# Kernel tuning notes

Measured on AMD Instinct MI355X. Metric: run time of the kernel, lower is better.

The kernel has to match this reference:

```python
import jax, jax.numpy as jnp
import numpy as np

N = 2500   # total_neurons
K = 50     # connections_per_neuron
T = 60     # temporal_sequence
F = 5      # input_features
H = 128    # lstm hidden_size
B = 512    # batch
GROUPS = [800, 700, 600, 400]  # support_resistance, trend_detection, pattern_recognition, volume_analysis


def _lstm_layer(x, Wih, Whh, bih, bhh):
    # x: [B, T, D]; PyTorch gate order (i, f, g, o); eval mode (no dropout)
    bs = x.shape[0]
    h0 = jnp.zeros((bs, H), x.dtype)

    def step(carry, xt):
        h, c = carry
        g = xt @ Wih.T + h @ Whh.T + bih + bhh
        i, f, gg, o = jnp.split(g, 4, axis=-1)
        c = jax.nn.sigmoid(f) * c + jax.nn.sigmoid(i) * jnp.tanh(gg)
        h = jax.nn.sigmoid(o) * jnp.tanh(c)
        return (h, c), h

    (h, c), ys = jax.lax.scan(step, (h0, h0), jnp.swapaxes(x, 0, 1))
    return jnp.swapaxes(ys, 0, 1), h


def _forward(x, W_ih0, W_hh0, b_ih0, b_hh0, W_ih1, W_hh1, b_ih1, b_hh1,
             fp_w1, fp_b1, fp_w2, fp_b2, conn_w, sens, thr,
             int_w1, int_b1, int_w2, int_b2, int_w3, int_b3,
             tw, tb, pw, pb, kw, kb, vw, vb, cw, cb, conn_idx):
    y0, _ = _lstm_layer(x, W_ih0, W_hh0, b_ih0, b_hh0)
    _, hlast = _lstm_layer(y0, W_ih1, W_hh1, b_ih1, b_hh1)        # hidden[-1]: [B, H]
    base = jnp.tanh(jax.nn.relu(hlast @ fp_w1.T + fp_b1) @ fp_w2.T + fp_b2)  # [B, 32]
    # all_activations = base repeated over N neurons; each neuron reduces its
    # K gathered activations (weighted) and the identical 32 feature dims to a scalar.
    feat_sum = base.sum(-1)                                        # [B]
    acts = jnp.broadcast_to(feat_sum[:, None], (x.shape[0], N))    # [B, N]
    gathered = acts[:, conn_idx]                                   # [B, N, K] irregular gather
    wi = jnp.einsum('bnk,nk->bn', gathered, conn_w)                # [B, N]
    pre = wi * sens
    o0 = GROUPS[0]; o1 = o0 + GROUPS[1]; o2 = o1 + GROUPS[2]
    neuron_out = jnp.concatenate([
        jax.nn.sigmoid(pre[:, :o0] - thr[:o0]),                    # support_resistance
        jnp.tanh(pre[:, o0:o1]),                                   # trend_detection
        jax.nn.relu(pre[:, o1:o2] - thr[o1:o2]),                   # pattern_recognition
        jax.nn.sigmoid(pre[:, o2:]),                               # volume_analysis
    ], axis=1)                                                     # [B, N]
    h1 = jax.nn.relu(neuron_out @ int_w1.T + int_b1)
    h2 = jax.nn.relu(h1 @ int_w2.T + int_b2)
    integrated = jnp.tanh(h2 @ int_w3.T + int_b3)                  # [B, 32]
    trend = integrated @ tw.T + tb                                 # [B, 3]
    patt = integrated @ pw.T + pb                                  # [B, 6]
    keyl = integrated @ kw.T + kb                                  # [B, 4]
    vol = integrated @ vw.T + vb                                   # [B, 1]
    conf = integrated @ cw.T + cb                                  # [B, 1]
    means = jnp.stack([neuron_out[:, :o0].mean(1), neuron_out[:, o0:o1].mean(1),
                       neuron_out[:, o1:o2].mean(1), neuron_out[:, o2:].mean(1)], axis=-1)
    # heads(15) + raw confidence(1) + overall_confidence(1) + specialty means(4) -> [B, 21]? no: 3+6+4+1+1+1+4 = 20
    return jnp.concatenate([trend, patt, keyl, vol, conf, jax.nn.sigmoid(conf), means], axis=-1)


def setup_inputs() -> dict:
    key = jax.random.key(0)
    ks = jax.random.split(key, 40)
    rn = lambda k, s, sc=0.1: jax.random.normal(k, s, dtype=jnp.float32) * sc
    inp = {}
    inp['x'] = jax.random.normal(ks[0], (B, T, F), dtype=jnp.float32)
    inp['W_ih0'] = rn(ks[1], (4 * H, F)); inp['W_hh0'] = rn(ks[2], (4 * H, H))
    inp['b_ih0'] = rn(ks[3], (4 * H,));   inp['b_hh0'] = rn(ks[4], (4 * H,))
    inp['W_ih1'] = rn(ks[5], (4 * H, H)); inp['W_hh1'] = rn(ks[6], (4 * H, H))
    inp['b_ih1'] = rn(ks[7], (4 * H,));   inp['b_hh1'] = rn(ks[8], (4 * H,))
    inp['fp_w1'] = rn(ks[9], (64, H));    inp['fp_b1'] = rn(ks[10], (64,))
    inp['fp_w2'] = rn(ks[11], (32, 64));  inp['fp_b2'] = rn(ks[12], (32,))
    inp['conn_w'] = rn(ks[13], (N, K))
    inp['sens'] = 1.0 + rn(ks[14], (N,))
    inp['thr'] = 0.6 + rn(ks[15], (N,))
    inp['int_w1'] = rn(ks[16], (256, N), 0.02); inp['int_b1'] = rn(ks[17], (256,))
    inp['int_w2'] = rn(ks[18], (64, 256));      inp['int_b2'] = rn(ks[19], (64,))
    inp['int_w3'] = rn(ks[20], (32, 64));       inp['int_b3'] = rn(ks[21], (32,))
    inp['tw'] = rn(ks[22], (3, 32)); inp['tb'] = rn(ks[23], (3,))
    inp['pw'] = rn(ks[24], (6, 32)); inp['pb'] = rn(ks[25], (6,))
    inp['kw'] = rn(ks[26], (4, 32)); inp['kb'] = rn(ks[27], (4,))
    inp['vw'] = rn(ks[28], (1, 32)); inp['vb'] = rn(ks[29], (1,))
    inp['cw'] = rn(ks[30], (1, 32)); inp['cb'] = rn(ks[31], (1,))
    inp['conn_idx'] = jax.random.randint(ks[32], (N, K), 0, N)
    return inp


def reference(x, W_ih0, W_hh0, b_ih0, b_hh0, W_ih1, W_hh1, b_ih1, b_hh1,
              fp_w1, fp_b1, fp_w2, fp_b2, conn_w, sens, thr,
              int_w1, int_b1, int_w2, int_b2, int_w3, int_b3,
              tw, tb, pw, pb, kw, kb, vw, vb, cw, cb, conn_idx):
    return _forward(x, W_ih0, W_hh0, b_ih0, b_hh0, W_ih1, W_hh1, b_ih1, b_hh1,
                    fp_w1, fp_b1, fp_w2, fp_b2, conn_w, sens, thr,
                    int_w1, int_b1, int_w2, int_b2, int_w3, int_b3,
                    tw, tb, pw, pb, kw, kb, vw, vb, cw, cb, conn_idx)
```

## Files before the change

kernel.cpp:

```cpp
#include <hip/hip_runtime.h>
#include <math.h>

#define NB   512
#define TT   60
#define FF   5
#define HH   128
#define G4   512
#define NN   2500
#define KK   50

#define O0 800
#define O1 1500
#define O2 2100

#define OFF_WA    0
#define OFF_WB    32768
#define OFF_WC    65536
#define OFF_W0T   98304
#define OFF_B0    100864
#define OFF_B1    101376
#define OFF_A     101888
#define OFF_FS    104388
#define OFF_NO    104900
#define OFF_MEANS (OFF_NO + NB*NN)
#define OFF_H1    (OFF_MEANS + 2048)

#define PREP_TOTAL 202692

typedef _Float16 half2v __attribute__((ext_vector_type(2)));

#if defined(__has_builtin)
#if __has_builtin(__builtin_amdgcn_fdot2)
#define DOT2(a, b, c) __builtin_amdgcn_fdot2((a), (b), (c), false)
#endif
#endif
#ifndef DOT2
#define DOT2(a, b, c) fmaf((float)(a).x, (float)(b).x, fmaf((float)(a).y, (float)(b).y, (c)))
#endif

union WU { unsigned u; half2v h; };
union HU { uint2 u2; half2v h[2]; };

__device__ __forceinline__ float sigf(float x) {
    return 1.0f / (1.0f + __expf(-x));
}
__device__ __forceinline__ float tanh_fast(float x) {
    float t = __expf(-2.0f * fabsf(x));
    float r = (1.0f - t) / (1.0f + t);
    return copysignf(r, x);
}

__global__ __launch_bounds__(256) void prep_kernel(
    const float* __restrict__ W_ih0, const float* __restrict__ W_hh0,
    const float* __restrict__ b_ih0, const float* __restrict__ b_hh0,
    const float* __restrict__ W_ih1, const float* __restrict__ W_hh1,
    const float* __restrict__ b_ih1, const float* __restrict__ b_hh1,
    const float* __restrict__ conn_w, const float* __restrict__ sens,
    float* __restrict__ ws)
{
    int i = blockIdx.x * 256 + threadIdx.x;
    if (i >= PREP_TOTAL) return;

    if (i < 196608) {
        int m = i >> 16;
        int v = i & 65535;
        int k2 = v >> 10, rem = v & 1023, j = rem >> 1, kk = rem & 1;
        const float* src = (m == 0) ? W_hh0 : (m == 1) ? W_ih1 : W_hh1;
        _Float16* dst = (_Float16*)(ws + (m == 0 ? OFF_WA : m == 1 ? OFF_WB : OFF_WC));
        dst[v] = (_Float16)src[j * HH + (k2 * 2 + kk)];
    } else if (i < 199168) {
        int v = i - 196608;
        int f = v >> 9, j = v & 511;
        ws[OFF_W0T + v] = W_ih0[j * FF + f];
    } else if (i < 199680) {
        int j = i - 199168;
        ws[OFF_B0 + j] = b_ih0[j] + b_hh0[j];
    } else if (i < 200192) {
        int j = i - 199680;
        ws[OFF_B1 + j] = b_ih1[j] + b_hh1[j];
    } else {
        int n = i - 200192;
        float s = 0.f;
        const float* cw = conn_w + n * KK;
        for (int k = 0; k < KK; ++k) s += cw[k];
        ws[OFF_A + n] = s * sens[n];
    }
}

__global__ __launch_bounds__(1024) void lstm_fused(
    const float* __restrict__ x,
    const float* __restrict__ ws_ro,
    const float* __restrict__ fp_w1, const float* __restrict__ fp_b1,
    const float* __restrict__ fp_w2, const float* __restrict__ fp_b2,
    float* __restrict__ feat_sum)
{
    __shared__ float xs[2][TT * FF + 4];
    __shared__ uint2 hb0h[HH / 2];
    __shared__ uint2 hb1h[HH / 2];
    __shared__ float gp[2 * G4 * 2];
    __shared__ float t1s[2][64];
    __shared__ float bss[2][32];

    const int tid = threadIdx.x;
    const int j = tid & 511;
    const int half = tid >> 9;
    const int brow = blockIdx.x * 2;

    for (int i = tid; i < 2 * TT * FF; i += 1024) {
        int r = i / (TT * FF), c = i % (TT * FF);
        xs[r][c] = x[(brow + r) * (TT * FF) + c];
    }
    if (tid < HH / 2) { hb0h[tid] = make_uint2(0u, 0u); hb1h[tid] = make_uint2(0u, 0u); }

    float w0r[FF];
    if (half == 0) {
#pragma unroll
        for (int f = 0; f < FF; ++f) w0r[f] = ws_ro[OFF_W0T + f * G4 + j];
    }
    const int ur = (tid >> 7) & 1, uk = tid & 127;
    float bi0 = 0.f, bf0 = 0.f, bg0 = 0.f, bo0 = 0.f;
    float bi1 = 0.f, bf1 = 0.f, bg1 = 0.f, bo1 = 0.f;
    if (tid < 256) {
        bi0 = ws_ro[OFF_B0 + uk];        bf0 = ws_ro[OFF_B0 + 128 + uk];
        bg0 = ws_ro[OFF_B0 + 256 + uk];  bo0 = ws_ro[OFF_B0 + 384 + uk];
        bi1 = ws_ro[OFF_B1 + uk];        bf1 = ws_ro[OFF_B1 + 128 + uk];
        bg1 = ws_ro[OFF_B1 + 256 + uk];  bo1 = ws_ro[OFF_B1 + 384 + uk];
    }
    float c0 = 0.f, c1 = 0.f;
    const int hwidx = (uk >> 1) * 4 + ur * 2 + (uk & 1);

    const unsigned* wAp = (const unsigned*)(ws_ro + OFF_WA) + (half << 5) * G4 + j;
    const unsigned* wCp = (const unsigned*)(ws_ro + (half ? OFF_WC : OFF_WB)) + j;
    const uint2* hCs = half ? hb1h : hb0h;
    float2* gpv = (float2*)gp;

    __syncthreads();

    for (int t = 0; t < TT; ++t) {
        float a0 = 0.f, a1 = 0.f;
#pragma unroll 8
        for (int k2 = 0; k2 < 32; ++k2) {
            WU w; w.u = wAp[k2 * G4];
            HU h; h.u2 = hb0h[(half << 5) + k2];
            a0 = DOT2(w.h, h.h[0], a0);
            a1 = DOT2(w.h, h.h[1], a1);
        }
        if (half == 0) {
            const float* xr0 = &xs[0][t * FF];
            const float* xr1 = &xs[1][t * FF];
#pragma unroll
            for (int f = 0; f < FF; ++f) {
                a0 = fmaf(w0r[f], xr0[f], a0);
                a1 = fmaf(w0r[f], xr1[f], a1);
            }
        }
        gpv[half * G4 + j] = make_float2(a0, a1);
        __syncthreads();

        if (tid < 256) {
            float ip = bi0 + gp[(uk) * 2 + ur]       + gp[(G4 + uk) * 2 + ur];
            float fp = bf0 + gp[(128 + uk) * 2 + ur] + gp[(G4 + 128 + uk) * 2 + ur];
            float gg = bg0 + gp[(256 + uk) * 2 + ur] + gp[(G4 + 256 + uk) * 2 + ur];
            float op = bo0 + gp[(384 + uk) * 2 + ur] + gp[(G4 + 384 + uk) * 2 + ur];
            c0 = sigf(fp) * c0 + sigf(ip) * tanh_fast(gg);
            ((_Float16*)hb0h)[hwidx] = (_Float16)(sigf(op) * tanh_fast(c0));
        }
        __syncthreads();

        a0 = 0.f; a1 = 0.f;
#pragma unroll 8
        for (int k2 = 0; k2 < 64; ++k2) {
            WU w; w.u = wCp[k2 * G4];
            HU h; h.u2 = hCs[k2];
            a0 = DOT2(w.h, h.h[0], a0);
            a1 = DOT2(w.h, h.h[1], a1);
        }
        gpv[half * G4 + j] = make_float2(a0, a1);
        __syncthreads();

        if (tid < 256) {
            float ip = bi1 + gp[(uk) * 2 + ur]       + gp[(G4 + uk) * 2 + ur];
            float fp = bf1 + gp[(128 + uk) * 2 + ur] + gp[(G4 + 128 + uk) * 2 + ur];
            float gg = bg1 + gp[(256 + uk) * 2 + ur] + gp[(G4 + 256 + uk) * 2 + ur];
            float op = bo1 + gp[(384 + uk) * 2 + ur] + gp[(G4 + 384 + uk) * 2 + ur];
            c1 = sigf(fp) * c1 + sigf(ip) * tanh_fast(gg);
            ((_Float16*)hb1h)[hwidx] = (_Float16)(sigf(op) * tanh_fast(c1));
        }
        __syncthreads();
    }

    if (tid < 128) {
        int r = tid >> 6, m = tid & 63;
        float acc = fp_b1[m];
        const float* wp = fp_w1 + m * HH;
        const _Float16* h1h = (const _Float16*)hb1h;
        for (int k = 0; k < HH; ++k)
            acc = fmaf(wp[k], (float)h1h[(k >> 1) * 4 + r * 2 + (k & 1)], acc);
        t1s[r][m] = fmaxf(acc, 0.f);
    }
    __syncthreads();
    if (tid < 64) {
        int r = tid >> 5, q = tid & 31;
        float acc = fp_b2[q];
        const float* wp = fp_w2 + q * 64;
        for (int m = 0; m < 64; ++m) acc = fmaf(wp[m], t1s[r][m], acc);
        bss[r][q] = tanh_fast(acc);
    }
    __syncthreads();
    if (tid < 2) {
        float s = 0.f;
        for (int q = 0; q < 32; ++q) s += bss[tid][q];
        feat_sum[brow + tid] = s;
    }
}

__global__ __launch_bounds__(256) void neuron_kernel(
    const float* __restrict__ feat_sum, const float* __restrict__ a,
    const float* __restrict__ thr,
    float* __restrict__ no, float* __restrict__ means)
{
    const int b = blockIdx.x;
    const float s = feat_sum[b];
    float g0 = 0.f, g1 = 0.f, g2 = 0.f, g3 = 0.f;
    for (int n = threadIdx.x; n < NN; n += 256) {
        float pre = s * a[n];
        float v;
        if (n < O0)        { v = sigf(pre - thr[n]);          g0 += v; }
        else if (n < O1)   { v = tanh_fast(pre);              g1 += v; }
        else if (n < O2)   { v = fmaxf(pre - thr[n], 0.f);    g2 += v; }
        else               { v = sigf(pre);                   g3 += v; }
        no[b * NN + n] = v;
    }
    __shared__ float red[4][256];
    red[0][threadIdx.x] = g0; red[1][threadIdx.x] = g1;
    red[2][threadIdx.x] = g2; red[3][threadIdx.x] = g3;
    __syncthreads();
    if (threadIdx.x < 4) {
        float acc = 0.f;
        for (int i = 0; i < 256; ++i) acc += red[threadIdx.x][i];
        const float inv[4] = {1.f / 800.f, 1.f / 700.f, 1.f / 600.f, 1.f / 400.f};
        means[b * 4 + threadIdx.x] = acc * inv[threadIdx.x];
    }
}

__global__ __launch_bounds__(256) void gemm_h1(
    const float* __restrict__ no,
    const float* __restrict__ int_w1,
    const float* __restrict__ int_b1,
    float* __restrict__ h1)
{
    __shared__ float As[32][33];
    __shared__ float Bs[32][33];
    const int b0 = blockIdx.x * 32;
    const int m0 = blockIdx.y * 32;
    const int tid = threadIdx.x;
    const int ty = tid >> 4, tx = tid & 15;
    const int li = tid >> 3;
    const int lj = (tid & 7) * 4;

    float acc00 = 0.f, acc01 = 0.f, acc10 = 0.f, acc11 = 0.f;

    for (int k0 = 0; k0 < NN; k0 += 32) {
        float4 av = make_float4(0.f, 0.f, 0.f, 0.f);
        if (k0 + lj < NN)
            av = *(const float4*)(no + (b0 + li) * NN + k0 + lj);
        As[li][lj + 0] = av.x; As[li][lj + 1] = av.y;
        As[li][lj + 2] = av.z; As[li][lj + 3] = av.w;

        float4 wv = make_float4(0.f, 0.f, 0.f, 0.f);
        if (k0 + lj < NN)
            wv = *(const float4*)(int_w1 + (m0 + li) * NN + k0 + lj);
        Bs[lj + 0][li] = wv.x; Bs[lj + 1][li] = wv.y;
        Bs[lj + 2][li] = wv.z; Bs[lj + 3][li] = wv.w;
        __syncthreads();

#pragma unroll 8
        for (int kk = 0; kk < 32; ++kk) {
            float a0 = As[ty * 2][kk],  a1 = As[ty * 2 + 1][kk];
            float w0 = Bs[kk][tx * 2],  w1 = Bs[kk][tx * 2 + 1];
            acc00 += a0 * w0; acc01 += a0 * w1;
            acc10 += a1 * w0; acc11 += a1 * w1;
        }
        __syncthreads();
    }
    const int bi = b0 + ty * 2, mj = m0 + tx * 2;
    h1[bi * 256 + mj]           = fmaxf(acc00 + int_b1[mj], 0.f);
    h1[bi * 256 + mj + 1]       = fmaxf(acc01 + int_b1[mj + 1], 0.f);
    h1[(bi + 1) * 256 + mj]     = fmaxf(acc10 + int_b1[mj], 0.f);
    h1[(bi + 1) * 256 + mj + 1] = fmaxf(acc11 + int_b1[mj + 1], 0.f);
}

__global__ __launch_bounds__(64) void tail_kernel(
    const float* __restrict__ h1,
    const float* __restrict__ int_w2, const float* __restrict__ int_b2,
    const float* __restrict__ int_w3, const float* __restrict__ int_b3,
    const float* __restrict__ tw, const float* __restrict__ tb,
    const float* __restrict__ pw, const float* __restrict__ pb,
    const float* __restrict__ kw, const float* __restrict__ kb,
    const float* __restrict__ vw, const float* __restrict__ vb,
    const float* __restrict__ cw, const float* __restrict__ cb,
    const float* __restrict__ means,
    float* __restrict__ out)
{
    const int b = blockIdx.x;
    const int lane = threadIdx.x;
    __shared__ float h2s[64];
    __shared__ float ints[32];
    __shared__ float outs[16];

    {
        float acc = int_b2[lane];
        const float* hp = h1 + b * 256;
        const float* wp = int_w2 + lane * 256;
        for (int m = 0; m < 256; ++m) acc += wp[m] * hp[m];
        h2s[lane] = fmaxf(acc, 0.f);
    }
    __syncthreads();
    if (lane < 32) {
        float acc = int_b3[lane];
        const float* wp = int_w3 + lane * 64;
        for (int m = 0; m < 64; ++m) acc += wp[m] * h2s[m];
        ints[lane] = tanh_fast(acc);
    }
    __syncthreads();
    if (lane < 15) {
        const float* wsel; float bsel;
        if (lane < 3)       { wsel = tw + lane * 32;       bsel = tb[lane]; }
        else if (lane < 9)  { wsel = pw + (lane - 3) * 32; bsel = pb[lane - 3]; }
        else if (lane < 13) { wsel = kw + (lane - 9) * 32; bsel = kb[lane - 9]; }
        else if (lane == 13){ wsel = vw;                   bsel = vb[0]; }
        else                { wsel = cw;                   bsel = cb[0]; }
        float acc = bsel;
        for (int q = 0; q < 32; ++q) acc += wsel[q] * ints[q];
        outs[lane] = acc;
    }
    __syncthreads();
    if (lane < 20) {
        float v;
        if (lane < 15)       v = outs[lane];
        else if (lane == 15) v = sigf(outs[14]);
        else                 v = means[b * 4 + (lane - 16)];
        out[b * 20 + lane] = v;
    }
}

extern "C" void kernel_launch(void* const* d_in, const int* in_sizes, int n_in,
                              void* d_out, int out_size, void* d_ws, size_t ws_size,
                              hipStream_t stream)
{
    const float* x      = (const float*)d_in[0];
    const float* W_ih0  = (const float*)d_in[1];
    const float* W_hh0  = (const float*)d_in[2];
    const float* b_ih0  = (const float*)d_in[3];
    const float* b_hh0  = (const float*)d_in[4];
    const float* W_ih1  = (const float*)d_in[5];
    const float* W_hh1  = (const float*)d_in[6];
    const float* b_ih1  = (const float*)d_in[7];
    const float* b_hh1  = (const float*)d_in[8];
    const float* fp_w1  = (const float*)d_in[9];
    const float* fp_b1  = (const float*)d_in[10];
    const float* fp_w2  = (const float*)d_in[11];
    const float* fp_b2  = (const float*)d_in[12];
    const float* conn_w = (const float*)d_in[13];
    const float* sens   = (const float*)d_in[14];
    const float* thr    = (const float*)d_in[15];
    const float* int_w1 = (const float*)d_in[16];
    const float* int_b1 = (const float*)d_in[17];
    const float* int_w2 = (const float*)d_in[18];
    const float* int_b2 = (const float*)d_in[19];
    const float* int_w3 = (const float*)d_in[20];
    const float* int_b3 = (const float*)d_in[21];
    const float* tw     = (const float*)d_in[22];
    const float* tb     = (const float*)d_in[23];
    const float* pw     = (const float*)d_in[24];
    const float* pb     = (const float*)d_in[25];
    const float* kw     = (const float*)d_in[26];
    const float* kb     = (const float*)d_in[27];
    const float* vw     = (const float*)d_in[28];
    const float* vb     = (const float*)d_in[29];
    const float* cw     = (const float*)d_in[30];
    const float* cb     = (const float*)d_in[31];

    float* ws = (float*)d_ws;
    float* out = (float*)d_out;

    prep_kernel<<<(PREP_TOTAL + 255) / 256, 256, 0, stream>>>(
        W_ih0, W_hh0, b_ih0, b_hh0, W_ih1, W_hh1, b_ih1, b_hh1,
        conn_w, sens, ws);

    lstm_fused<<<NB / 2, 1024, 0, stream>>>(
        x, ws, fp_w1, fp_b1, fp_w2, fp_b2, ws + OFF_FS);

    neuron_kernel<<<NB, 256, 0, stream>>>(
        ws + OFF_FS, ws + OFF_A, thr, ws + OFF_NO, ws + OFF_MEANS);

    {
        dim3 grid(NB / 32, 256 / 32);
        gemm_h1<<<grid, 256, 0, stream>>>(
            ws + OFF_NO, int_w1, int_b1, ws + OFF_H1);
    }

    tail_kernel<<<NB, 64, 0, stream>>>(
        ws + OFF_H1, int_w2, int_b2, int_w3, int_b3,
        tw, tb, pw, pb, kw, kb, vw, vb, cw, cb,
        ws + OFF_MEANS, out);
}
```

Baseline: 380.9 us.

## Repartition LSTM matvec into 4-way K-split with gate-pair tiles and register-resident weights

```diff
diff --git a/kernel.cpp b/kernel.cpp
--- a/kernel.cpp
+++ b/kernel.cpp
@@ -39,7 +39,6 @@
 #endif
 
 union WU { unsigned u; half2v h; };
-union HU { uint2 u2; half2v h[2]; };
 
 __device__ __forceinline__ float sigf(float x) {
     return 1.0f / (1.0f + __expf(-x));
@@ -48,6 +47,19 @@
     float t = __expf(-2.0f * fabsf(x));
     float r = (1.0f - t) / (1.0f + t);
     return copysignf(r, x);
+}
+
+__device__ __forceinline__ void dot_pair(unsigned wj0, unsigned wj1,
+                                         unsigned hr0, unsigned hr1,
+                                         float& a00, float& a01,
+                                         float& a10, float& a11)
+{
+    WU w0; w0.u = wj0;  WU w1; w1.u = wj1;
+    WU h0; h0.u = hr0;  WU h1; h1.u = hr1;
+    a00 = DOT2(w0.h, h0.h, a00);
+    a01 = DOT2(w0.h, h1.h, a01);
+    a10 = DOT2(w1.h, h0.h, a10);
+    a11 = DOT2(w1.h, h1.h, a11);
 }
 
 __global__ __launch_bounds__(256) void prep_kernel(
@@ -64,7 +76,9 @@
     if (i < 196608) {
         int m = i >> 16;
         int v = i & 65535;
-        int k2 = v >> 10, rem = v & 1023, j = rem >> 1, kk = rem & 1;
+        int k2 = v >> 10, rem = v & 1023;
+        int jp = rem >> 2, jj = (rem >> 1) & 1, kk = rem & 1;
+        int j = jp * 2 + jj;
         const float* src = (m == 0) ? W_hh0 : (m == 1) ? W_ih1 : W_hh1;
         _Float16* dst = (_Float16*)(ws + (m == 0 ? OFF_WA : m == 1 ? OFF_WB : OFF_WC));
         dst[v] = (_Float16)src[j * HH + (k2 * 2 + kk)];
@@ -95,28 +109,25 @@
     float* __restrict__ feat_sum)
 {
     __shared__ float xs[2][TT * FF + 4];
-    __shared__ uint2 hb0h[HH / 2];
-    __shared__ uint2 hb1h[HH / 2];
-    __shared__ float gp[2 * G4 * 2];
+    __shared__ __align__(16) uint2 hb0h[HH / 2];
+    __shared__ __align__(16) uint2 hb1h[HH / 2];
+    __shared__ float gp[4 * 256 * 4];
+    __shared__ float w0s[2560];
     __shared__ float t1s[2][64];
     __shared__ float bss[2][32];
 
     const int tid = threadIdx.x;
-    const int j = tid & 511;
-    const int half = tid >> 9;
+    const int jp = tid & 255;
+    const int q = tid >> 8;
     const int brow = blockIdx.x * 2;
 
     for (int i = tid; i < 2 * TT * FF; i += 1024) {
         int r = i / (TT * FF), c = i % (TT * FF);
         xs[r][c] = x[(brow + r) * (TT * FF) + c];
     }
+    for (int i = tid; i < 2560; i += 1024) w0s[i] = ws_ro[OFF_W0T + i];
     if (tid < HH / 2) { hb0h[tid] = make_uint2(0u, 0u); hb1h[tid] = make_uint2(0u, 0u); }
 
-    float w0r[FF];
-    if (half == 0) {
-#pragma unroll
-        for (int f = 0; f < FF; ++f) w0r[f] = ws_ro[OFF_W0T + f * G4 + j];
-    }
     const int ur = (tid >> 7) & 1, uk = tid & 127;
     float bi0 = 0.f, bf0 = 0.f, bg0 = 0.f, bo0 = 0.f;
     float bi1 = 0.f, bf1 = 0.f, bg1 = 0.f, bo1 = 0.f;
@@ -129,62 +140,81 @@
     float c0 = 0.f, c1 = 0.f;
     const int hwidx = (uk >> 1) * 4 + ur * 2 + (uk & 1);
 
-    const unsigned* wAp = (const unsigned*)(ws_ro + OFF_WA) + (half << 5) * G4 + j;
-    const unsigned* wCp = (const unsigned*)(ws_ro + (half ? OFF_WC : OFF_WB)) + j;
-    const uint2* hCs = half ? hb1h : hb0h;
-    float2* gpv = (float2*)gp;
+    const uint2* wBp = (const uint2*)(ws_ro + OFF_WB) + (q * 16) * 256 + jp;
+    const uint2* wCp = (const uint2*)(ws_ro + OFF_WC) + (q * 16) * 256 + jp;
+    uint2 wBr[16], wCr[16];
+#pragma unroll
+    for (int i = 0; i < 16; ++i) { wBr[i] = wBp[i * 256]; wCr[i] = wCp[i * 256]; }
+
+    const uint2* wAq = (const uint2*)(ws_ro + OFF_WA) + (q * 16) * 256 + jp;
+    const uint4* h0q = (const uint4*)hb0h + q * 8;
+    const uint4* h1q = (const uint4*)hb1h + q * 8;
+    float4* gpv4 = (float4*)gp;
 
     __syncthreads();
 
     for (int t = 0; t < TT; ++t) {
-        float a0 = 0.f, a1 = 0.f;
-#pragma unroll 8
-        for (int k2 = 0; k2 < 32; ++k2) {
-            WU w; w.u = wAp[k2 * G4];
-            HU h; h.u2 = hb0h[(half << 5) + k2];
-            a0 = DOT2(w.h, h.h[0], a0);
-            a1 = DOT2(w.h, h.h[1], a1);
+        float a00 = 0.f, a01 = 0.f, a10 = 0.f, a11 = 0.f;
+#pragma unroll
+        for (int i = 0; i < 8; ++i) {
+            uint4 h4 = h0q[i];
+            uint2 wv0 = wAq[(2 * i) * 256];
+            uint2 wv1 = wAq[(2 * i + 1) * 256];
+            dot_pair(wv0.x, wv0.y, h4.x, h4.y, a00, a01, a10, a11);
+            dot_pair(wv1.x, wv1.y, h4.z, h4.w, a00, a01, a10, a11);
         }
-        if (half == 0) {
-            const float* xr0 = &xs[0][t * FF];
-            const float* xr1 = &xs[1][t * FF];
+        gpv4[q * 256 + jp] = make_float4(a00, a01, a10, a11);
+        __syncthreads();
+
+        if (tid < 256) {
+            float gi = bi0, gf = bf0, gg = bg0, go = bo0;
+#pragma unroll
+            for (int qq = 0; qq < 4; ++qq) {
+                int base = qq * 1024 + (uk >> 1) * 4 + (uk & 1) * 2 + ur;
+                gi += gp[base];
+                gf += gp[base + 256];
+                gg += gp[base + 512];
+                go += gp[base + 768];
+            }
+            const float* xr = &xs[ur][t * FF];
 #pragma unroll
             for (int f = 0; f < FF; ++f) {
-                a0 = fmaf(w0r[f], xr0[f], a0);
-                a1 = fmaf(w0r[f], xr1[f], a1);
+                float xf = xr[f];
+                gi = fmaf(w0s[f * G4 + uk],       xf, gi);
+                gf = fmaf(w0s[f * G4 + 128 + uk], xf, gf);
+                gg = fmaf(w0s[f * G4 + 256 + uk], xf, gg);
+                go = fmaf(w0s[f * G4 + 384 + uk], xf, go);
             }
+            c0 = sigf(gf) * c0 + sigf(gi) * tanh_fast(gg);
+            ((_Float16*)hb0h)[hwidx] = (_Float16)(sigf(go) * tanh_fast(c0));
         }
-        gpv[half * G4 + j] = make_float2(a0, a1);
+        __syncthreads();
+
+        a00 = 0.f; a01 = 0.f; a10 = 0.f; a11 = 0.f;
+#pragma unroll
+        for (int i = 0; i < 8; ++i) {
+            uint4 h04 = h0q[i];
+            uint4 h14 = h1q[i];
+            dot_pair(wBr[2 * i].x,     wBr[2 * i].y,     h04.x, h04.y, a00, a01, a10, a11);
+            dot_pair(wBr[2 * i + 1].x, wBr[2 * i + 1].y, h04.z, h04.w, a00, a01, a10, a11);
+            dot_pair(wCr[2 * i].x,     wCr[2 * i].y,     h14.x, h14.y, a00, a01, a10, a11);
+            dot_pair(wCr[2 * i + 1].x, wCr[2 * i + 1].y, h14.z, h14.w, a00, a01, a10, a11);
+        }
+        gpv4[q * 256 + jp] = make_float4(a00, a01, a10, a11);
         __syncthreads();
 
         if (tid < 256) {
-            float ip = bi0 + gp[(uk) * 2 + ur]       + gp[(G4 + uk) * 2 + ur];
-            float fp = bf0 + gp[(128 + uk) * 2 + ur] + gp[(G4 + 128 + uk) * 2 + ur];
-            float gg = bg0 + gp[(256 + uk) * 2 + ur] + gp[(G4 + 256 + uk) * 2 + ur];
-            float op = bo0 + gp[(384 + uk) * 2 + ur] + gp[(G4 + 384 + uk) * 2 + ur];
-            c0 = sigf(fp) * c0 + sigf(ip) * tanh_fast(gg);
-            ((_Float16*)hb0h)[hwidx] = (_Float16)(sigf(op) * tanh_fast(c0));
-        }
-        __syncthreads();
-
-        a0 = 0.f; a1 = 0.f;
-#pragma unroll 8
-        for (int k2 = 0; k2 < 64; ++k2) {
-            WU w; w.u = wCp[k2 * G4];
-            HU h; h.u2 = hCs[k2];
-            a0 = DOT2(w.h, h.h[0], a0);
-            a1 = DOT2(w.h, h.h[1], a1);
-        }
-        gpv[half * G4 + j] = make_float2(a0, a1);
-        __syncthreads();
-
-        if (tid < 256) {
-            float ip = bi1 + gp[(uk) * 2 + ur]       + gp[(G4 + uk) * 2 + ur];
-            float fp = bf1 + gp[(128 + uk) * 2 + ur] + gp[(G4 + 128 + uk) * 2 + ur];
-            float gg = bg1 + gp[(256 + uk) * 2 + ur] + gp[(G4 + 256 + uk) * 2 + ur];
-            float op = bo1 + gp[(384 + uk) * 2 + ur] + gp[(G4 + 384 + uk) * 2 + ur];
-            c1 = sigf(fp) * c1 + sigf(ip) * tanh_fast(gg);
-            ((_Float16*)hb1h)[hwidx] = (_Float16)(sigf(op) * tanh_fast(c1));
+            float gi = bi1, gf = bf1, gg = bg1, go = bo1;
+#pragma unroll
+            for (int qq = 0; qq < 4; ++qq) {
+                int base = qq * 1024 + (uk >> 1) * 4 + (uk & 1) * 2 + ur;
+                gi += gp[base];
+                gf += gp[base + 256];
+                gg += gp[base + 512];
+                go += gp[base + 768];
+            }
+            c1 = sigf(gf) * c1 + sigf(gi) * tanh_fast(gg);
+            ((_Float16*)hb1h)[hwidx] = (_Float16)(sigf(go) * tanh_fast(c1));
         }
         __syncthreads();
     }
@@ -200,16 +230,16 @@
     }
     __syncthreads();
     if (tid < 64) {
-        int r = tid >> 5, q = tid & 31;
-        float acc = fp_b2[q];
-        const float* wp = fp_w2 + q * 64;
+        int r = tid >> 5, qq = tid & 31;
+        float acc = fp_b2[qq];
+        const float* wp = fp_w2 + qq * 64;
         for (int m = 0; m < 64; ++m) acc = fmaf(wp[m], t1s[r][m], acc);
-        bss[r][q] = tanh_fast(acc);
+        bss[r][qq] = tanh_fast(acc);
     }
     __syncthreads();
     if (tid < 2) {
         float s = 0.f;
-        for (int q = 0; q < 32; ++q) s += bss[tid][q];
+        for (int qq = 0; qq < 32; ++qq) s += bss[tid][qq];
         feat_sum[brow + tid] = s;
     }
 }
@@ -331,7 +361,7 @@
         else if (lane == 13){ wsel = vw;                   bsel = vb[0]; }
         else                { wsel = cw;                   bsel = cb[0]; }
         float acc = bsel;
-        for (int q = 0; q < 32; ++q) acc += wsel[q] * ints[q];
+        for (int qq = 0; qq < 32; ++qq) acc += wsel[qq] * ints[qq];
         outs[lane] = acc;
     }
     __syncthreads();
```

Measured after the change: 474.1 us. 1.24x slower.
